# Performance work log

Hardware: AMD Instinct MI355X
Metric: run time of the kernel (lower is better)

Reference implementation:

```python
import jax, jax.numpy as jnp
import numpy as np

N_NODES = 30000
DIM = 128
N_T = 6
N_EDGES = 480000
NEG_SLOPE = 0.2  # GATConv default leaky_relu slope


def _gat(x, src, dst, W, att_src, att_dst, b):
    # PyG GATConv, heads=1, add_self_loops=True, eval mode (no dropout).
    n = x.shape[0]
    loops = jnp.arange(n)
    src = jnp.concatenate([src, loops])
    dst = jnp.concatenate([dst, loops])
    h = x @ W                              # [N, D]
    a_s = h @ att_src                      # [N]
    a_d = h @ att_dst                      # [N]
    e = jax.nn.leaky_relu(a_s[src] + a_d[dst], NEG_SLOPE)   # [E+N]
    m = jax.ops.segment_max(e, dst, num_segments=n)
    ex = jnp.exp(e - m[dst])
    denom = jax.ops.segment_sum(ex, dst, num_segments=n)
    alpha = ex / denom[dst]
    out = jax.ops.segment_sum(h[src] * alpha[:, None], dst, num_segments=n)
    return out + b


def _sage(x, src, dst, Wl, bl, Wr, br):
    # PyG SAGEConv, mean aggregation, root_weight=True.
    n = x.shape[0]
    agg = jax.ops.segment_sum(x[src], dst, num_segments=n)
    cnt = jax.ops.segment_sum(jnp.ones_like(src, dtype=x.dtype), dst, num_segments=n)
    mean = agg / jnp.maximum(cnt, 1.0)[:, None]
    return mean @ Wl + bl + x @ Wr + br


def setup_inputs() -> dict:
    key = jax.random.key(0)
    ks = jax.random.split(key, 16)
    sc = 0.1
    inp = {
        "s": jax.random.randint(ks[0], (1024,), 0, N_NODES),
        "t_s": jax.random.randint(ks[1], (1024,), 0, N_T),
        "t_e": jax.random.randint(ks[2], (1024,), 0, N_T),
        "edge_index": jax.random.randint(ks[3], (N_T, 3, 2, N_EDGES), 0, N_NODES),
        "embed_weight": jax.random.normal(ks[4], (N_NODES, DIM), jnp.float32),
        "W_p": jax.random.normal(ks[5], (DIM, DIM), jnp.float32) * sc,
        "att_src_p": jax.random.normal(ks[6], (DIM,), jnp.float32) * sc,
        "att_dst_p": jax.random.normal(ks[7], (DIM,), jnp.float32) * sc,
        "b_p": jnp.zeros((DIM,), jnp.float32),
        "W_c": jax.random.normal(ks[8], (DIM, DIM), jnp.float32) * sc,
        "att_src_c": jax.random.normal(ks[9], (DIM,), jnp.float32) * sc,
        "att_dst_c": jax.random.normal(ks[10], (DIM,), jnp.float32) * sc,
        "b_c": jnp.zeros((DIM,), jnp.float32),
        "W_l": jax.random.normal(ks[11], (DIM, DIM), jnp.float32) * sc,
        "b_l": jnp.zeros((DIM,), jnp.float32),
        "W_r": jax.random.normal(ks[12], (DIM, DIM), jnp.float32) * sc,
        "b_r": jnp.zeros((DIM,), jnp.float32),
    }
    return inp


def reference(s, t_s, t_e, edge_index, embed_weight,
              W_p, att_src_p, att_dst_p, b_p,
              W_c, att_src_c, att_dst_c, b_c,
              W_l, b_l, W_r, b_r):
    outs = []
    for t in range(N_T):  # fixed small number of timesteps
        ei = edge_index[t]
        gp = _gat(embed_weight, ei[0, 0], ei[0, 1], W_p, att_src_p, att_dst_p, b_p)
        gc = _gat(embed_weight, ei[1, 0], ei[1, 1], W_c, att_src_c, att_dst_c, b_c)
        sg = _sage(embed_weight, ei[2, 0], ei[2, 1], W_l, b_l, W_r, b_r)
        outs.append((gp + gc + sg) / 3.0)  # HeteroConv aggr='mean'
    skill_embs = jnp.stack(outs)           # [n, N, D]
    return skill_embs[:, s, :]             # [n, |s|, D]
```

## Files before the change

kernel.cpp:

```cpp
#include <hip/hip_runtime.h>
#include <hip/hip_bf16.h>

#define NN 30000
#define DIM 128
#define NT 6
#define NE 480000
#define NSLOT 1024
#define NSEG (NT*3*NSLOT)
#define SEGCAP 96
#define NBM ((NN+31)/32)
#define QCAP 2048
#define HB 2048

typedef __attribute__((ext_vector_type(8))) short bf16x8;
typedef __attribute__((ext_vector_type(4))) float f32x4;

__device__ __forceinline__ float lrelu(float x){ return x > 0.f ? x : 0.2f*x; }
__device__ __forceinline__ unsigned short f2b(float f){
    unsigned u = __float_as_uint(f);
    u = (u + 0x7FFFu + ((u>>16)&1u)) >> 16;
    return (unsigned short)u;
}
__device__ __forceinline__ float b2f(unsigned short b){
    return __uint_as_float(((unsigned)b)<<16);
}
__device__ __forceinline__ float blo(unsigned p){ return b2f((unsigned short)(p & 0xFFFF)); }
__device__ __forceinline__ float bhi(unsigned p){ return b2f((unsigned short)(p >> 16)); }
__device__ __forceinline__ unsigned hsh(int v){ return ((unsigned)v*2654435761u >> 21) & (HB-1); }

__global__ void k_prep(const float* __restrict__ Wp, const float* __restrict__ Wc,
        const float* __restrict__ Wl, const float* __restrict__ Wr,
        const float* __restrict__ aspv, const float* __restrict__ adpv,
        const float* __restrict__ ascv, const float* __restrict__ adcv,
        const int* __restrict__ s, unsigned* __restrict__ bm,
        unsigned* __restrict__ hmap, int* __restrict__ rep, int* __restrict__ cnt,
        float* __restrict__ wa, unsigned short* __restrict__ WT4){
    int m = blockIdx.x, t = threadIdx.x;
    if (m >= 5){
        int b = m - 5;
        int per = (NSEG + 7)/8;
        for (int j = b*per + t; j < (b+1)*per && j < NSEG; j += 256) cnt[j] = 0;
        return;
    }
    if (m == 4){
        __shared__ int hk[HB];
        __shared__ int hv[HB];
        __shared__ unsigned bms[NBM];
        for (int j = t; j < HB; j += 256){ hk[j] = -1; hv[j] = 1<<30; }
        for (int j = t; j < NBM; j += 256) bms[j] = 0u;
        __syncthreads();
        for (int i = t; i < NSLOT; i += 256){
            int v = s[i];
            unsigned idx = hsh(v);
            while (true){
                int old = atomicCAS(&hk[idx], -1, v);
                if (old == -1 || old == v){ atomicMin(&hv[idx], i); break; }
                idx = (idx+1)&(HB-1);
            }
            atomicOr(&bms[v>>5], 1u << (v&31));
        }
        __syncthreads();
        for (int j = t; j < NBM; j += 256) bm[j] = bms[j];
        for (int j = t; j < HB; j += 256){
            int k = hk[j];
            hmap[j] = (k < 0) ? 0xFFFFFFFFu : (((unsigned)k << 10) | (unsigned)hv[j]);
        }
        for (int i = t; i < NSLOT; i += 256){
            int v = s[i];
            unsigned idx = hsh(v);
            while (hk[idx] != v) idx = (idx+1)&(HB-1);
            rep[i] = hv[idx];
        }
        return;
    }
    const float* W = (m==0) ? Wp : (m==1) ? Wc : (m==2) ? Wl : Wr;
    unsigned short* WT = WT4 + (size_t)m*DIM*DIM;
    if (m < 2 && t < DIM){
        const float* avs = m ? ascv : aspv;
        const float* avd = m ? adcv : adpv;
        float* wab = wa + m*2*DIM;
        float sv = 0.f, dv = 0.f;
        for (int n = 0; n < DIM; n++){
            float w = W[t*DIM + n];
            sv += w*avs[n]; dv += w*avd[n];
        }
        wab[t] = sv; wab[DIM + t] = dv;
    }
    for (int j = t; j < DIM*DIM; j += blockDim.x){
        int n = j >> 7, k = j & 127;
        WT[n*DIM + k] = f2b(W[k*DIM + n]);
    }
}

__global__ __launch_bounds__(256) void k_cast(const float* __restrict__ X,
        const float* __restrict__ wa, unsigned* __restrict__ Xbf,
        float* __restrict__ asp, float* __restrict__ adp,
        float* __restrict__ asc, float* __restrict__ adc){
    int gw = (blockIdx.x*blockDim.x + threadIdx.x) >> 6;
    int lane = threadIdx.x & 63;
    if (gw >= NN) return;
    float2 x = *(const float2*)&X[(size_t)gw*DIM + lane*2];
    Xbf[(size_t)gw*64 + lane] = (unsigned)f2b(x.x) | ((unsigned)f2b(x.y) << 16);
    float sp = x.x*wa[2*lane]     + x.y*wa[2*lane+1];
    float dp = x.x*wa[128+2*lane] + x.y*wa[128+2*lane+1];
    float sc = x.x*wa[256+2*lane] + x.y*wa[256+2*lane+1];
    float dc = x.x*wa[384+2*lane] + x.y*wa[384+2*lane+1];
    #pragma unroll
    for (int off = 32; off; off >>= 1){
        sp += __shfl_xor(sp, off); dp += __shfl_xor(dp, off);
        sc += __shfl_xor(sc, off); dc += __shfl_xor(dc, off);
    }
    if (lane == 0){ asp[gw] = sp; adp[gw] = dp; asc[gw] = sc; adc[gw] = dc; }
}

__global__ __launch_bounds__(256) void k_build(const int* __restrict__ EI,
        const unsigned* __restrict__ bm, const unsigned* __restrict__ hmap,
        int* __restrict__ cnt, int* __restrict__ csr){
    __shared__ unsigned bms[NBM];
    __shared__ unsigned q[QCAP];
    __shared__ int qn;
    for (int j = threadIdx.x; j < NBM; j += 256) bms[j] = bm[j];
    if (threadIdx.x == 0) qn = 0;
    __syncthreads();
    const int Q = NE/4;
    const int G = gridDim.x*blockDim.x;
    int row = blockIdx.y;
    const int4* dstp = (const int4*)(EI + (size_t)(2*row+1)*NE);
    const int4* srcp = (const int4*)(EI + (size_t)(2*row)*NE);
    int tid = blockIdx.x*blockDim.x + threadIdx.x;
    int lane = threadIdx.x & 63;

    int4 d[4]; int ix[4]; bool va[4];
    #pragma unroll
    for (int u = 0; u < 4; u++){
        ix[u] = tid + u*G;
        va[u] = ix[u] < Q;
        d[u] = va[u] ? dstp[ix[u]] : make_int4(0,0,0,0);
    }
    unsigned mk[4];
    #pragma unroll
    for (int u = 0; u < 4; u++){
        unsigned m0 = va[u] ? ((bms[d[u].x>>5] >> (d[u].x&31)) & 1u) : 0u;
        unsigned m1 = va[u] ? ((bms[d[u].y>>5] >> (d[u].y&31)) & 1u) : 0u;
        unsigned m2 = va[u] ? ((bms[d[u].z>>5] >> (d[u].z&31)) & 1u) : 0u;
        unsigned m3 = va[u] ? ((bms[d[u].w>>5] >> (d[u].w&31)) & 1u) : 0u;
        mk[u] = m0 | (m1<<1) | (m2<<2) | (m3<<3);
    }
    int4 sv[4];
    #pragma unroll
    for (int u = 0; u < 4; u++)
        if (mk[u]) sv[u] = srcp[ix[u]];
    #pragma unroll
    for (int u = 0; u < 4; u++){
        #pragma unroll
        for (int c = 0; c < 4; c++){
            bool p = (mk[u] >> c) & 1u;
            unsigned long long bal = __ballot(p);
            if (bal){
                int cntw = __popcll(bal);
                int base = 0;
                if (lane == 0) base = atomicAdd(&qn, cntw);
                base = __shfl(base, 0);
                if (p){
                    int dv = (c==0)?d[u].x:(c==1)?d[u].y:(c==2)?d[u].z:d[u].w;
                    int so = (c==0)?sv[u].x:(c==1)?sv[u].y:(c==2)?sv[u].z:sv[u].w;
                    int pos = base + __popcll(bal & ((1ull<<lane)-1ull));
                    if (pos < QCAP) q[pos] = ((unsigned)dv<<15) | (unsigned)so;
                }
            }
        }
    }
    __syncthreads();
    int base = row*NSLOT;
    int tot = qn; if (tot > QCAP) tot = QCAP;
    for (int j = threadIdx.x; j < tot; j += 256){
        unsigned e = q[j];
        int dst = (int)(e >> 15);
        int src = (int)(e & 32767u);
        unsigned idx = hsh(dst);
        unsigned he;
        while (((he = hmap[idx]) >> 10) != (unsigned)dst) idx = (idx+1)&(HB-1);
        int sl = (int)(he & 1023u);
        int p = atomicAdd(&cnt[base+sl], 1);
        if (p < SEGCAP) csr[(size_t)(base+sl)*SEGCAP + p] = src;
    }
}

__global__ __launch_bounds__(256) void k_aggr(const unsigned* __restrict__ Xbf,
        const float* __restrict__ asp, const float* __restrict__ adp,
        const float* __restrict__ asc, const float* __restrict__ adc,
        const int* __restrict__ s, const int* __restrict__ cnt, const int* __restrict__ csr,
        unsigned* __restrict__ aggb){
    int gw = (blockIdx.x*blockDim.x + threadIdx.x) >> 6;
    int lane = threadIdx.x & 63;
    if (gw >= NSEG) return;
    int slot = gw & (NSLOT-1);
    int tg = gw >> 10;
    int g = tg % 3;
    int n = cnt[gw]; if (n > SEGCAP) n = SEGCAP;
    const int* lst = csr + (size_t)gw*SEGCAP;
    int src0 = (lane < n) ? lst[lane] : 0;
    int src1 = (64+lane < n) ? lst[64+lane] : 0;
    int n0 = n < 64 ? n : 64;
    float w0, w1, wself = 0.f, scale;
    int v = -1;
    if (g == 2){
        w0 = (lane < n) ? 1.f : 0.f;
        w1 = (64+lane < n) ? 1.f : 0.f;
        scale = 1.f / (float)(n > 0 ? n : 1);
    } else {
        const float* as = g ? asc : asp;
        const float* ad = g ? adc : adp;
        v = s[slot];
        float adv = ad[v];
        float eself = lrelu(as[v] + adv);
        float e0 = (lane < n)    ? lrelu(as[src0]+adv) : -3e38f;
        float e1 = (64+lane < n) ? lrelu(as[src1]+adv) : -3e38f;
        float m = fmaxf(eself, fmaxf(e0, e1));
        #pragma unroll
        for (int off = 32; off; off >>= 1) m = fmaxf(m, __shfl_xor(m, off));
        w0 = (lane < n)    ? __expf(e0 - m) : 0.f;
        w1 = (64+lane < n) ? __expf(e1 - m) : 0.f;
        float ds = w0 + w1;
        #pragma unroll
        for (int off = 32; off; off >>= 1) ds += __shfl_xor(ds, off);
        wself = __expf(eself - m);
        scale = 1.f / (wself + ds);
    }
    float a0 = 0.f, a1 = 0.f;
    int j = 0;
    for (; j+7 < n0; j += 8){
        int   si[8]; float qi[8]; unsigned ki[8];
        #pragma unroll
        for (int u = 0; u < 8; u++){ si[u] = __shfl(src0, j+u); qi[u] = __shfl(w0, j+u); }
        #pragma unroll
        for (int u = 0; u < 8; u++) ki[u] = Xbf[(size_t)si[u]*64 + lane];
        #pragma unroll
        for (int u = 0; u < 8; u++){ a0 += qi[u]*blo(ki[u]); a1 += qi[u]*bhi(ki[u]); }
    }
    for (; j+3 < n0; j += 4){
        int s0=__shfl(src0,j), s1=__shfl(src0,j+1), s2=__shfl(src0,j+2), s3=__shfl(src0,j+3);
        float q0=__shfl(w0,j), q1=__shfl(w0,j+1), q2=__shfl(w0,j+2), q3=__shfl(w0,j+3);
        unsigned k0=Xbf[(size_t)s0*64+lane];
        unsigned k1=Xbf[(size_t)s1*64+lane];
        unsigned k2=Xbf[(size_t)s2*64+lane];
        unsigned k3=Xbf[(size_t)s3*64+lane];
        a0 += q0*blo(k0) + q1*blo(k1) + q2*blo(k2) + q3*blo(k3);
        a1 += q0*bhi(k0) + q1*bhi(k1) + q2*bhi(k2) + q3*bhi(k3);
    }
    for (; j < n0; j++){
        int sj=__shfl(src0,j);
        float qj=__shfl(w0,j);
        unsigned pk=Xbf[(size_t)sj*64+lane];
        a0 += qj*blo(pk); a1 += qj*bhi(pk);
    }
    for (j = 64; j < n; j++){
        int sj=__shfl(src1,j-64);
        float qj=__shfl(w1,j-64);
        unsigned pk=Xbf[(size_t)sj*64+lane];
        a0 += qj*blo(pk); a1 += qj*bhi(pk);
    }
    if (g < 2){
        unsigned pk = Xbf[(size_t)v*64 + lane];
        a0 += wself*blo(pk); a1 += wself*bhi(pk);
    }
    aggb[(size_t)gw*64 + lane] =
        (unsigned)f2b(a0*scale) | ((unsigned)f2b(a1*scale) << 16);
}

__global__ __launch_bounds__(256) void k_sgemm(const unsigned* __restrict__ aggb,
        const unsigned* __restrict__ Xbf, const unsigned short* __restrict__ WT4,
        const int* __restrict__ s,
        float* __restrict__ aggOut, float* __restrict__ xWr){
    int task = (blockIdx.x >= 288);
    int blk  = task ? (blockIdx.x - 288) : blockIdx.x;
    int wsel = task ? 3 : ((blk >> 4) % 3);
    const unsigned short* WT = WT4 + (size_t)wsel*DIM*DIM;
    float* out = task ? xWr : aggOut;
    int rows = task ? NSLOT : NSEG;
    int wid = threadIdx.x >> 6, lane = threadIdx.x & 63;
    int r0 = blk*64 + wid*16;
    int ar = r0 + (lane & 15); if (ar > rows-1) ar = rows-1;
    int g = lane >> 4;
    const unsigned short* Arow = task
        ? (const unsigned short*)(Xbf + (size_t)s[ar]*64)
        : (const unsigned short*)(aggb + (size_t)ar*64);
    bf16x8 Af[4];
    #pragma unroll
    for (int ks = 0; ks < 4; ks++)
        Af[ks] = *(const bf16x8*)&Arow[ks*32 + g*8];
    int cl = lane & 15;
    #pragma unroll
    for (int ct = 0; ct < 8; ct++){
        f32x4 acc = {0.f,0.f,0.f,0.f};
        int bcol = ct*16 + cl;
        #pragma unroll
        for (int ks = 0; ks < 4; ks++){
            bf16x8 bF = *(const bf16x8*)&WT[bcol*DIM + ks*32 + g*8];
            acc = __builtin_amdgcn_mfma_f32_16x16x32_bf16(Af[ks], bF, acc, 0, 0, 0);
        }
        #pragma unroll
        for (int r = 0; r < 4; r++){
            int row = r0 + g*4 + r;
            if (row < rows) out[(size_t)row*DIM + bcol] = acc[r];
        }
    }
}

__global__ void k_gather(const int* __restrict__ rep,
                         const float* __restrict__ aggOut, const float* __restrict__ xWr,
                         const float* __restrict__ bp, const float* __restrict__ bc,
                         const float* __restrict__ bl, const float* __restrict__ br,
                         float* __restrict__ out){
    int i = blockIdx.x*blockDim.x + threadIdx.x;
    if (i >= NT*NSLOT*DIM) return;
    int d = i & 127;
    int r = (i >> 7) & (NSLOT-1);
    int t = i >> 17;
    int rp = rep[r];
    size_t base = ((size_t)(t*3)*NSLOT + rp)*DIM + d;
    out[i] = (aggOut[base] + aggOut[base + NSLOT*DIM] + aggOut[base + 2*NSLOT*DIM]
              + xWr[(size_t)rp*DIM + d]
              + bp[d] + bc[d] + bl[d] + br[d]) * (1.f/3.f);
}

extern "C" void kernel_launch(void* const* d_in, const int* in_sizes, int n_in,
                              void* d_out, int out_size, void* d_ws, size_t ws_size,
                              hipStream_t stream) {
    const int*   s    = (const int*)d_in[0];
    const int*   EI   = (const int*)d_in[3];
    const float* X    = (const float*)d_in[4];
    const float* Wp   = (const float*)d_in[5];
    const float* aspv = (const float*)d_in[6];
    const float* adpv = (const float*)d_in[7];
    const float* bp   = (const float*)d_in[8];
    const float* Wc   = (const float*)d_in[9];
    const float* ascv = (const float*)d_in[10];
    const float* adcv = (const float*)d_in[11];
    const float* bc   = (const float*)d_in[12];
    const float* Wl   = (const float*)d_in[13];
    const float* bl   = (const float*)d_in[14];
    const float* Wr   = (const float*)d_in[15];
    const float* br   = (const float*)d_in[16];
    float* out = (float*)d_out;

    char* w = (char*)d_ws;
    unsigned* Xbf = (unsigned*)w; w += (size_t)NN*64*4;
    unsigned short* WT4 = (unsigned short*)w; w += (size_t)4*DIM*DIM*2;
    float* wa  = (float*)w; w += (size_t)4*DIM*4;
    float* asp = (float*)w; w += (size_t)NN*4;
    float* adp = (float*)w; w += (size_t)NN*4;
    float* asc = (float*)w; w += (size_t)NN*4;
    float* adc = (float*)w; w += (size_t)NN*4;
    unsigned* bm = (unsigned*)w; w += (size_t)((NBM+3)&~3)*4;
    unsigned* hmap = (unsigned*)w; w += (size_t)HB*4;
    int* rep  = (int*)w; w += (size_t)NSLOT*4;
    int* cnt  = (int*)w; w += (size_t)NSEG*4;
    int* csr  = (int*)w; w += (size_t)NSEG*SEGCAP*4;
    unsigned* aggb = (unsigned*)w; w += (size_t)NSEG*64*4;
    float* aggOut = (float*)w; w += (size_t)NSEG*DIM*4;
    float* xWr = (float*)w; w += (size_t)NSLOT*DIM*4;

    k_prep   <<<13, 256, 0, stream>>>(Wp, Wc, Wl, Wr, aspv, adpv, ascv, adcv,
                                      s, bm, hmap, rep, cnt, wa, WT4);
    k_cast   <<<(NN+3)/4, 256, 0, stream>>>(X, wa, Xbf, asp, adp, asc, adc);
    k_build  <<<dim3(118, 18), 256, 0, stream>>>(EI, bm, hmap, cnt, csr);
    k_aggr   <<<NSEG/4, 256, 0, stream>>>(Xbf, asp, adp, asc, adc, s, cnt, csr, aggb);
    k_sgemm  <<<304, 256, 0, stream>>>(aggb, Xbf, WT4, s, aggOut, xWr);
    k_gather <<<NT*NSLOT*DIM/256, 256, 0, stream>>>(rep, aggOut, xWr, bp, bc, bl, br, out);
}
```

Before: 84.68 us.

## Fuse cast with CSR build and aggregation with GEMM into single kernels

Cast/attention-score computation and CSR build now run as disjoint block ranges of one launch, since neither depends on the other. Aggregation and the projection GEMM are fused so each block aggregates 16 segments into an LDS bf16 tile and multiplies it by the weight directly, which removes the aggb round trip through global memory. The Wr projection runs as extra blocks in the same launch. This cuts two launches and an intermediate buffer. In exchange, each block serialises four segments per wave before a barrier, so aggregation parallelism per block drops and load imbalance can grow.

Measured after the change: 75.43 us. 10.9% less time.

```diff
diff --git a/kernel.cpp b/kernel.cpp
--- a/kernel.cpp
+++ b/kernel.cpp
@@ -11,6 +11,9 @@
 #define NBM ((NN+31)/32)
 #define QCAP 2048
 #define HB 2048
+#define NBUILD 2124
+#define NCAST 876
+#define NAGG (NSEG/16)
 
 typedef __attribute__((ext_vector_type(8))) short bf16x8;
 typedef __attribute__((ext_vector_type(4))) float f32x4;
@@ -92,43 +95,47 @@
     }
 }
 
-__global__ __launch_bounds__(256) void k_cast(const float* __restrict__ X,
-        const float* __restrict__ wa, unsigned* __restrict__ Xbf,
+__global__ __launch_bounds__(256) void k_castbuild(
+        const float* __restrict__ X, const float* __restrict__ wa,
+        unsigned* __restrict__ Xbf,
         float* __restrict__ asp, float* __restrict__ adp,
-        float* __restrict__ asc, float* __restrict__ adc){
-    int gw = (blockIdx.x*blockDim.x + threadIdx.x) >> 6;
-    int lane = threadIdx.x & 63;
-    if (gw >= NN) return;
-    float2 x = *(const float2*)&X[(size_t)gw*DIM + lane*2];
-    Xbf[(size_t)gw*64 + lane] = (unsigned)f2b(x.x) | ((unsigned)f2b(x.y) << 16);
-    float sp = x.x*wa[2*lane]     + x.y*wa[2*lane+1];
-    float dp = x.x*wa[128+2*lane] + x.y*wa[128+2*lane+1];
-    float sc = x.x*wa[256+2*lane] + x.y*wa[256+2*lane+1];
-    float dc = x.x*wa[384+2*lane] + x.y*wa[384+2*lane+1];
-    #pragma unroll
-    for (int off = 32; off; off >>= 1){
-        sp += __shfl_xor(sp, off); dp += __shfl_xor(dp, off);
-        sc += __shfl_xor(sc, off); dc += __shfl_xor(dc, off);
-    }
-    if (lane == 0){ asp[gw] = sp; adp[gw] = dp; asc[gw] = sc; adc[gw] = dc; }
-}
-
-__global__ __launch_bounds__(256) void k_build(const int* __restrict__ EI,
+        float* __restrict__ asc, float* __restrict__ adc,
+        const int* __restrict__ EI,
         const unsigned* __restrict__ bm, const unsigned* __restrict__ hmap,
         int* __restrict__ cnt, int* __restrict__ csr){
     __shared__ unsigned bms[NBM];
     __shared__ unsigned q[QCAP];
     __shared__ int qn;
+    int bx = blockIdx.x;
+    int lane = threadIdx.x & 63;
+    int wib = threadIdx.x >> 6;
+    if (bx < NCAST){
+        for (int node = bx*4 + wib; node < NN; node += NCAST*4){
+            float2 x = *(const float2*)&X[(size_t)node*DIM + lane*2];
+            Xbf[(size_t)node*64 + lane] = (unsigned)f2b(x.x) | ((unsigned)f2b(x.y) << 16);
+            float sp = x.x*wa[2*lane]     + x.y*wa[2*lane+1];
+            float dp = x.x*wa[128+2*lane] + x.y*wa[128+2*lane+1];
+            float sc = x.x*wa[256+2*lane] + x.y*wa[256+2*lane+1];
+            float dc = x.x*wa[384+2*lane] + x.y*wa[384+2*lane+1];
+            #pragma unroll
+            for (int off = 32; off; off >>= 1){
+                sp += __shfl_xor(sp, off); dp += __shfl_xor(dp, off);
+                sc += __shfl_xor(sc, off); dc += __shfl_xor(dc, off);
+            }
+            if (lane == 0){ asp[node]=sp; adp[node]=dp; asc[node]=sc; adc[node]=dc; }
+        }
+        return;
+    }
+    int bb = bx - NCAST;
+    int row = bb / 118, bxx = bb - row*118;
     for (int j = threadIdx.x; j < NBM; j += 256) bms[j] = bm[j];
     if (threadIdx.x == 0) qn = 0;
     __syncthreads();
     const int Q = NE/4;
-    const int G = gridDim.x*blockDim.x;
-    int row = blockIdx.y;
+    const int G = 118*256;
     const int4* dstp = (const int4*)(EI + (size_t)(2*row+1)*NE);
     const int4* srcp = (const int4*)(EI + (size_t)(2*row)*NE);
-    int tid = blockIdx.x*blockDim.x + threadIdx.x;
-    int lane = threadIdx.x & 63;
+    int tid = bxx*256 + threadIdx.x;
 
     int4 d[4]; int ix[4]; bool va[4];
     #pragma unroll
@@ -186,123 +193,141 @@
     }
 }
 
-__global__ __launch_bounds__(256) void k_aggr(const unsigned* __restrict__ Xbf,
+__global__ __launch_bounds__(256) void k_aggemm(const unsigned* __restrict__ Xbf,
         const float* __restrict__ asp, const float* __restrict__ adp,
         const float* __restrict__ asc, const float* __restrict__ adc,
         const int* __restrict__ s, const int* __restrict__ cnt, const int* __restrict__ csr,
-        unsigned* __restrict__ aggb){
-    int gw = (blockIdx.x*blockDim.x + threadIdx.x) >> 6;
+        const unsigned short* __restrict__ WT4,
+        float* __restrict__ aggOut, float* __restrict__ xWr){
+    __shared__ unsigned tile[16][72];
+    int bx = blockIdx.x;
     int lane = threadIdx.x & 63;
-    if (gw >= NSEG) return;
-    int slot = gw & (NSLOT-1);
-    int tg = gw >> 10;
+    int wib = threadIdx.x >> 6;
+    if (bx >= NAGG){
+        int blk = bx - NAGG;
+        const unsigned short* WT = WT4 + (size_t)3*DIM*DIM;
+        int r0 = blk*64 + wib*16;
+        int ar = r0 + (lane & 15); if (ar > NSLOT-1) ar = NSLOT-1;
+        int g4 = lane >> 4;
+        const unsigned short* Arow = (const unsigned short*)(Xbf + (size_t)s[ar]*64);
+        bf16x8 Af[4];
+        #pragma unroll
+        for (int ks = 0; ks < 4; ks++)
+            Af[ks] = *(const bf16x8*)&Arow[ks*32 + g4*8];
+        int cl = lane & 15;
+        #pragma unroll
+        for (int ct = 0; ct < 8; ct++){
+            f32x4 acc = {0.f,0.f,0.f,0.f};
+            int bcol = ct*16 + cl;
+            #pragma unroll
+            for (int ks = 0; ks < 4; ks++){
+                bf16x8 bF = *(const bf16x8*)&WT[bcol*DIM + ks*32 + g4*8];
+                acc = __builtin_amdgcn_mfma_f32_16x16x32_bf16(Af[ks], bF, acc, 0, 0, 0);
+            }
+            #pragma unroll
+            for (int r = 0; r < 4; r++){
+                int rw = r0 + g4*4 + r;
+                if (rw < NSLOT) xWr[(size_t)rw*DIM + bcol] = acc[r];
+            }
+        }
+        return;
+    }
+    int base_gw = bx*16;
+    int tg = base_gw >> 10;
     int g = tg % 3;
-    int n = cnt[gw]; if (n > SEGCAP) n = SEGCAP;
-    const int* lst = csr + (size_t)gw*SEGCAP;
-    int src0 = (lane < n) ? lst[lane] : 0;
-    int src1 = (64+lane < n) ? lst[64+lane] : 0;
-    int n0 = n < 64 ? n : 64;
-    float w0, w1, wself = 0.f, scale;
-    int v = -1;
-    if (g == 2){
-        w0 = (lane < n) ? 1.f : 0.f;
-        w1 = (64+lane < n) ? 1.f : 0.f;
-        scale = 1.f / (float)(n > 0 ? n : 1);
-    } else {
-        const float* as = g ? asc : asp;
-        const float* ad = g ? adc : adp;
-        v = s[slot];
-        float adv = ad[v];
-        float eself = lrelu(as[v] + adv);
-        float e0 = (lane < n)    ? lrelu(as[src0]+adv) : -3e38f;
-        float e1 = (64+lane < n) ? lrelu(as[src1]+adv) : -3e38f;
-        float m = fmaxf(eself, fmaxf(e0, e1));
-        #pragma unroll
-        for (int off = 32; off; off >>= 1) m = fmaxf(m, __shfl_xor(m, off));
-        w0 = (lane < n)    ? __expf(e0 - m) : 0.f;
-        w1 = (64+lane < n) ? __expf(e1 - m) : 0.f;
-        float ds = w0 + w1;
-        #pragma unroll
-        for (int off = 32; off; off >>= 1) ds += __shfl_xor(ds, off);
-        wself = __expf(eself - m);
-        scale = 1.f / (wself + ds);
-    }
-    float a0 = 0.f, a1 = 0.f;
-    int j = 0;
-    for (; j+7 < n0; j += 8){
-        int   si[8]; float qi[8]; unsigned ki[8];
-        #pragma unroll
-        for (int u = 0; u < 8; u++){ si[u] = __shfl(src0, j+u); qi[u] = __shfl(w0, j+u); }
-        #pragma unroll
-        for (int u = 0; u < 8; u++) ki[u] = Xbf[(size_t)si[u]*64 + lane];
-        #pragma unroll
-        for (int u = 0; u < 8; u++){ a0 += qi[u]*blo(ki[u]); a1 += qi[u]*bhi(ki[u]); }
-    }
-    for (; j+3 < n0; j += 4){
-        int s0=__shfl(src0,j), s1=__shfl(src0,j+1), s2=__shfl(src0,j+2), s3=__shfl(src0,j+3);
-        float q0=__shfl(w0,j), q1=__shfl(w0,j+1), q2=__shfl(w0,j+2), q3=__shfl(w0,j+3);
-        unsigned k0=Xbf[(size_t)s0*64+lane];
-        unsigned k1=Xbf[(size_t)s1*64+lane];
-        unsigned k2=Xbf[(size_t)s2*64+lane];
-        unsigned k3=Xbf[(size_t)s3*64+lane];
-        a0 += q0*blo(k0) + q1*blo(k1) + q2*blo(k2) + q3*blo(k3);
-        a1 += q0*bhi(k0) + q1*bhi(k1) + q2*bhi(k2) + q3*bhi(k3);
-    }
-    for (; j < n0; j++){
-        int sj=__shfl(src0,j);
-        float qj=__shfl(w0,j);
-        unsigned pk=Xbf[(size_t)sj*64+lane];
-        a0 += qj*blo(pk); a1 += qj*bhi(pk);
-    }
-    for (j = 64; j < n; j++){
-        int sj=__shfl(src1,j-64);
-        float qj=__shfl(w1,j-64);
-        unsigned pk=Xbf[(size_t)sj*64+lane];
-        a0 += qj*blo(pk); a1 += qj*bhi(pk);
-    }
-    if (g < 2){
-        unsigned pk = Xbf[(size_t)v*64 + lane];
-        a0 += wself*blo(pk); a1 += wself*bhi(pk);
-    }
-    aggb[(size_t)gw*64 + lane] =
-        (unsigned)f2b(a0*scale) | ((unsigned)f2b(a1*scale) << 16);
-}
-
-__global__ __launch_bounds__(256) void k_sgemm(const unsigned* __restrict__ aggb,
-        const unsigned* __restrict__ Xbf, const unsigned short* __restrict__ WT4,
-        const int* __restrict__ s,
-        float* __restrict__ aggOut, float* __restrict__ xWr){
-    int task = (blockIdx.x >= 288);
-    int blk  = task ? (blockIdx.x - 288) : blockIdx.x;
-    int wsel = task ? 3 : ((blk >> 4) % 3);
-    const unsigned short* WT = WT4 + (size_t)wsel*DIM*DIM;
-    float* out = task ? xWr : aggOut;
-    int rows = task ? NSLOT : NSEG;
-    int wid = threadIdx.x >> 6, lane = threadIdx.x & 63;
-    int r0 = blk*64 + wid*16;
-    int ar = r0 + (lane & 15); if (ar > rows-1) ar = rows-1;
-    int g = lane >> 4;
-    const unsigned short* Arow = task
-        ? (const unsigned short*)(Xbf + (size_t)s[ar]*64)
-        : (const unsigned short*)(aggb + (size_t)ar*64);
+    const float* as = (g==1) ? asc : asp;
+    const float* ad = (g==1) ? adc : adp;
+    for (int k = 0; k < 4; k++){
+        int segi = wib*4 + k;
+        int gw = base_gw + segi;
+        int slot = gw & (NSLOT-1);
+        int n = cnt[gw]; if (n > SEGCAP) n = SEGCAP;
+        const int* lst = csr + (size_t)gw*SEGCAP;
+        int src0 = (lane < n) ? lst[lane] : 0;
+        int src1 = (64+lane < n) ? lst[64+lane] : 0;
+        int n0 = n < 64 ? n : 64;
+        float w0, w1, wself = 0.f, scale;
+        int v = -1;
+        if (g == 2){
+            w0 = (lane < n) ? 1.f : 0.f;
+            w1 = (64+lane < n) ? 1.f : 0.f;
+            scale = 1.f / (float)(n > 0 ? n : 1);
+        } else {
+            v = s[slot];
+            float adv = ad[v];
+            float eself = lrelu(as[v] + adv);
+            float e0 = (lane < n)    ? lrelu(as[src0]+adv) : -3e38f;
+            float e1 = (64+lane < n) ? lrelu(as[src1]+adv) : -3e38f;
+            float m = fmaxf(eself, fmaxf(e0, e1));
+            #pragma unroll
+            for (int off = 32; off; off >>= 1) m = fmaxf(m, __shfl_xor(m, off));
+            w0 = (lane < n)    ? __expf(e0 - m) : 0.f;
+            w1 = (64+lane < n) ? __expf(e1 - m) : 0.f;
+            float ds = w0 + w1;
+            #pragma unroll
+            for (int off = 32; off; off >>= 1) ds += __shfl_xor(ds, off);
+            wself = __expf(eself - m);
+            scale = 1.f / (wself + ds);
+        }
+        float a0 = 0.f, a1 = 0.f;
+        int j = 0;
+        for (; j+7 < n0; j += 8){
+            int   si[8]; float qi[8]; unsigned ki[8];
+            #pragma unroll
+            for (int u = 0; u < 8; u++){ si[u] = __shfl(src0, j+u); qi[u] = __shfl(w0, j+u); }
+            #pragma unroll
+            for (int u = 0; u < 8; u++) ki[u] = Xbf[(size_t)si[u]*64 + lane];
+            #pragma unroll
+            for (int u = 0; u < 8; u++){ a0 += qi[u]*blo(ki[u]); a1 += qi[u]*bhi(ki[u]); }
+        }
+        for (; j+3 < n0; j += 4){
+            int s0=__shfl(src0,j), s1=__shfl(src0,j+1), s2=__shfl(src0,j+2), s3=__shfl(src0,j+3);
+            float q0=__shfl(w0,j), q1=__shfl(w0,j+1), q2=__shfl(w0,j+2), q3=__shfl(w0,j+3);
+            unsigned k0=Xbf[(size_t)s0*64+lane];
+            unsigned k1=Xbf[(size_t)s1*64+lane];
+            unsigned k2=Xbf[(size_t)s2*64+lane];
+            unsigned k3=Xbf[(size_t)s3*64+lane];
+            a0 += q0*blo(k0) + q1*blo(k1) + q2*blo(k2) + q3*blo(k3);
+            a1 += q0*bhi(k0) + q1*bhi(k1) + q2*bhi(k2) + q3*bhi(k3);
+        }
+        for (; j < n0; j++){
+            int sj=__shfl(src0,j);
+            float qj=__shfl(w0,j);
+            unsigned pk=Xbf[(size_t)sj*64+lane];
+            a0 += qj*blo(pk); a1 += qj*bhi(pk);
+        }
+        for (j = 64; j < n; j++){
+            int sj=__shfl(src1,j-64);
+            float qj=__shfl(w1,j-64);
+            unsigned pk=Xbf[(size_t)sj*64+lane];
+            a0 += qj*blo(pk); a1 += qj*bhi(pk);
+        }
+        if (g < 2){
+            unsigned pk = Xbf[(size_t)v*64 + lane];
+            a0 += wself*blo(pk); a1 += wself*bhi(pk);
+        }
+        tile[segi][lane] = (unsigned)f2b(a0*scale) | ((unsigned)f2b(a1*scale) << 16);
+    }
+    __syncthreads();
+    const unsigned short* WT = WT4 + (size_t)g*DIM*DIM;
+    int r = lane & 15, g4 = lane >> 4;
     bf16x8 Af[4];
     #pragma unroll
     for (int ks = 0; ks < 4; ks++)
-        Af[ks] = *(const bf16x8*)&Arow[ks*32 + g*8];
-    int cl = lane & 15;
-    #pragma unroll
-    for (int ct = 0; ct < 8; ct++){
+        Af[ks] = *(const bf16x8*)&tile[r][ks*16 + g4*4];
+    #pragma unroll
+    for (int ct = 0; ct < 2; ct++){
         f32x4 acc = {0.f,0.f,0.f,0.f};
-        int bcol = ct*16 + cl;
+        int bcol = wib*32 + ct*16 + r;
         #pragma unroll
         for (int ks = 0; ks < 4; ks++){
-            bf16x8 bF = *(const bf16x8*)&WT[bcol*DIM + ks*32 + g*8];
+            bf16x8 bF = *(const bf16x8*)&WT[bcol*DIM + ks*32 + g4*8];
             acc = __builtin_amdgcn_mfma_f32_16x16x32_bf16(Af[ks], bF, acc, 0, 0, 0);
         }
         #pragma unroll
-        for (int r = 0; r < 4; r++){
-            int row = r0 + g*4 + r;
-            if (row < rows) out[(size_t)row*DIM + bcol] = acc[r];
+        for (int rr = 0; rr < 4; rr++){
+            int segrow = g4*4 + rr;
+            aggOut[(size_t)(base_gw + segrow)*DIM + bcol] = acc[rr];
         }
     }
 }
@@ -357,15 +382,14 @@
     int* rep  = (int*)w; w += (size_t)NSLOT*4;
     int* cnt  = (int*)w; w += (size_t)NSEG*4;
     int* csr  = (int*)w; w += (size_t)NSEG*SEGCAP*4;
-    unsigned* aggb = (unsigned*)w; w += (size_t)NSEG*64*4;
     float* aggOut = (float*)w; w += (size_t)NSEG*DIM*4;
     float* xWr = (float*)w; w += (size_t)NSLOT*DIM*4;
 
-    k_prep   <<<13, 256, 0, stream>>>(Wp, Wc, Wl, Wr, aspv, adpv, ascv, adcv,
-                                      s, bm, hmap, rep, cnt, wa, WT4);
-    k_cast   <<<(NN+3)/4, 256, 0, stream>>>(X, wa, Xbf, asp, adp, asc, adc);
-    k_build  <<<dim3(118, 18), 256, 0, stream>>>(EI, bm, hmap, cnt, csr);
-    k_aggr   <<<NSEG/4, 256, 0, stream>>>(Xbf, asp, adp, asc, adc, s, cnt, csr, aggb);
-    k_sgemm  <<<304, 256, 0, stream>>>(aggb, Xbf, WT4, s, aggOut, xWr);
-    k_gather <<<NT*NSLOT*DIM/256, 256, 0, stream>>>(rep, aggOut, xWr, bp, bc, bl, br, out);
-}
+    k_prep      <<<13, 256, 0, stream>>>(Wp, Wc, Wl, Wr, aspv, adpv, ascv, adcv,
+                                         s, bm, hmap, rep, cnt, wa, WT4);
+    k_castbuild <<<NCAST+NBUILD, 256, 0, stream>>>(X, wa, Xbf, asp, adp, asc, adc,
+                                                   EI, bm, hmap, cnt, csr);
+    k_aggemm    <<<NAGG+16, 256, 0, stream>>>(Xbf, asp, adp, asc, adc, s, cnt, csr,
+                                              WT4, aggOut, xWr);
+    k_gather    <<<NT*NSLOT*DIM/256, 256, 0, stream>>>(rep, aggOut, xWr, bp, bc, bl, br, out);
+}
```
